# Kernel optimization log

Hardware: AMD Instinct MI355X
Metric: run time of the kernel (lower is better)

The kernel has to match this reference:

```python
import jax, jax.numpy as jnp
import numpy as np

D = 1024  # input_size == context_size

def setup_inputs() -> dict:
    key = jax.random.key(0)
    ks = jax.random.split(key, 8)
    B, S = 16, 4096
    s = 1.0 / np.sqrt(D)
    return {
        "x": jax.random.normal(ks[0], (B, S, D), dtype=jnp.float32),
        "context": jax.random.normal(ks[1], (B, D), dtype=jnp.float32),
        "W_in": jax.random.uniform(ks[2], (D, D), jnp.float32, -s, s),
        "b_in": jax.random.uniform(ks[3], (D,), jnp.float32, -s, s),
        "W_ctx": jax.random.uniform(ks[4], (D, D), jnp.float32, -s, s),
        "b_ctx": jax.random.uniform(ks[5], (D,), jnp.float32, -s, s),
        "w_att": jax.random.uniform(ks[6], (D,), jnp.float32, -s, s),
        "b_att": jax.random.uniform(ks[7], (), jnp.float32, -s, s),
    }

def reference(x, context, W_in, b_in, W_ctx, b_ctx, w_att, b_att):
    # projected_input: [B,S,D]; projected_context: [B,D] broadcast over S
    pi = jnp.einsum('bsd,ed->bse', x, W_in) + b_in
    pc = jnp.einsum('bd,ed->be', context, W_ctx) + b_ctx
    h = jnp.tanh(pi + pc[:, None, :])                      # [B,S,D]
    scores = jnp.einsum('bsd,d->bs', h, w_att) + b_att      # [B,S]
    weights = jax.nn.softmax(scores, axis=1)                # [B,S]
    context_vector = jnp.einsum('bs,bsd->bd', weights, x)   # [B,D]
    # dropout is identity in eval mode
    return context_vector
```

## Files before the change

kernel.cpp:

```cpp
#include <hip/hip_runtime.h>
#include <hip/hip_bf16.h>
#include <math.h>

#define NB 16
#define NS 4096
#define ND 1024
#define NM (NB * NS)

#define WS_T       0
#define WS_SCORES  16384
#define WS_WEIGHTS (WS_SCORES + NB * NS)
#define WS_SHARED  (WS_WEIGHTS + NB * NS)
#define WS_XBF16   (WS_SHARED + 524288)
#define WS_SPART   (WS_XBF16 + 33554432)
#define WS_NEED    (((size_t)WS_SPART + 524288) * 4)

typedef short v8s __attribute__((ext_vector_type(8)));
typedef float v4f __attribute__((ext_vector_type(4)));
typedef unsigned short ushort;

#define G_AS __attribute__((address_space(1)))
#define L_AS __attribute__((address_space(3)))

__device__ __forceinline__ ushort f2bf(float f) {
    __hip_bfloat16 h = __float2bfloat16(f);
    return *reinterpret_cast<ushort*>(&h);
}

__device__ __forceinline__ float bf2f(ushort u) {
    return __uint_as_float(((unsigned)u) << 16);
}

__device__ __forceinline__ float fast_tanh(float x) {
    float e = __expf(2.0f * x);
    return 1.0f - 2.0f / (e + 1.0f);
}

__global__ __launch_bounds__(256) void convw_kernel(const float* __restrict__ W,
                                                    ushort* __restrict__ Wb) {
    int flat = blockIdx.x * 256 + threadIdx.x;
#pragma unroll
    for (int j = 0; j < 2; ++j) {
        int idx = flat + j * 131072;
        float4 v = ((const float4*)W)[idx];
        ushort4 o;
        o.x = f2bf(v.x); o.y = f2bf(v.y); o.z = f2bf(v.z); o.w = f2bf(v.w);
        ((ushort4*)Wb)[idx] = o;
    }
}

__global__ __launch_bounds__(256) void convx_kernel(const float* __restrict__ x,
                                                    ushort* __restrict__ xb) {
    size_t base = (size_t)blockIdx.x * 256 + threadIdx.x;
#pragma unroll
    for (int i = 0; i < 16; ++i) {
        size_t idx8 = base + (size_t)i * 524288;
        float4 a = ((const float4*)x)[idx8 * 2];
        float4 c = ((const float4*)x)[idx8 * 2 + 1];
        v8s o;
        o[0] = (short)f2bf(a.x); o[1] = (short)f2bf(a.y);
        o[2] = (short)f2bf(a.z); o[3] = (short)f2bf(a.w);
        o[4] = (short)f2bf(c.x); o[5] = (short)f2bf(c.y);
        o[6] = (short)f2bf(c.z); o[7] = (short)f2bf(c.w);
        ((v8s*)xb)[idx8] = o;
    }
}

__global__ __launch_bounds__(256) void tvec_kernel(const float* __restrict__ context,
                                                   const float* __restrict__ W_ctx,
                                                   const float* __restrict__ b_in,
                                                   const float* __restrict__ b_ctx,
                                                   float* __restrict__ t) {
    __shared__ float ctx[ND];
    int b = blockIdx.y;
    int tid = threadIdx.x;
    for (int i = tid; i < ND; i += 256) ctx[i] = context[b * ND + i];
    __syncthreads();
    int e = blockIdx.x * 64 + (tid >> 2);
    int kq = tid & 3;
    const float4* wr = (const float4*)(W_ctx + (size_t)e * ND + kq * 256);
    const float4* cr = (const float4*)(ctx + kq * 256);
    float acc = 0.f;
#pragma unroll 4
    for (int k = 0; k < 64; ++k) {
        float4 w = wr[k];
        float4 c = cr[k];
        acc += c.x * w.x + c.y * w.y + c.z * w.z + c.w * w.w;
    }
    acc += __shfl_xor(acc, 1);
    acc += __shfl_xor(acc, 2);
    if (kq == 0) t[b * ND + e] = acc + b_in[e] + b_ctx[e];
}

__global__ __launch_bounds__(512) void scores_tile_kernel(const ushort* __restrict__ xbf,
                                                          const ushort* __restrict__ Wb,
                                                          const float* __restrict__ t,
                                                          const float* __restrict__ w_att,
                                                          float* __restrict__ spart) {
    __shared__ ushort As[2][16384];
    __shared__ ushort Bs[2][16384];
    __shared__ float red[8][128];

    int tid = threadIdx.x;
    int o = blockIdx.x;
    int xcd = o & 7, idx = o >> 3;
    int ct = idx & 3;
    int rt = xcd * 32 + (idx >> 2);
    int row0 = rt << 8;
    int e0 = ct << 8;
    int b = row0 >> 12;

    int scol = ((tid & 7) ^ ((tid >> 3) & 7)) * 8;
    const ushort* gA = xbf + (size_t)(row0 + (tid >> 3)) * ND + scol;
    const ushort* gB = Wb + (size_t)(e0 + (tid >> 3)) * ND + scol;

    int wid = tid >> 6, l = tid & 63;
    int l15 = l & 15, kq4 = l >> 4;
    int l7 = l15 & 7;
    int WM = (wid >> 2) * 128;
    int WN = (wid & 3) * 64;

    v4f acc[8][4];
#pragma unroll
    for (int i = 0; i < 8; ++i)
#pragma unroll
        for (int j = 0; j < 4; ++j) acc[i][j] = (v4f)(0.f);

#define STAGE_A(SB, H, KO)                                                                              \
    {                                                                                                   \
        __builtin_amdgcn_global_load_lds((const G_AS void*)(gA + (size_t)(H) * 128 * ND + (KO)),        \
                                         (L_AS void*)&As[SB][((H) * 1024 + tid) * 8], 16, 0, 0);        \
        __builtin_amdgcn_global_load_lds((const G_AS void*)(gA + (size_t)((H) * 128 + 64) * ND + (KO)), \
                                         (L_AS void*)&As[SB][((H) * 1024 + 512 + tid) * 8], 16, 0, 0);  \
    }
#define STAGE_B(SB, H, KO)                                                                              \
    {                                                                                                   \
        __builtin_amdgcn_global_load_lds((const G_AS void*)(gB + (size_t)(H) * 128 * ND + (KO)),        \
                                         (L_AS void*)&Bs[SB][((H) * 1024 + tid) * 8], 16, 0, 0);        \
        __builtin_amdgcn_global_load_lds((const G_AS void*)(gB + (size_t)((H) * 128 + 64) * ND + (KO)), \
                                         (L_AS void*)&Bs[SB][((H) * 1024 + 512 + tid) * 8], 16, 0, 0);  \
    }

#define PHASE(BUF, KK, MH, STMT)                                                                   \
    {                                                                                              \
        STMT;                                                                                      \
        const int kswz = (((KK) * 4 + kq4) ^ l7) * 8;                                              \
        v8s af[4], bf[4];                                                                          \
        _Pragma("unroll") for (int j = 0; j < 4; ++j)                                              \
            af[j] = *(const v8s*)&As[BUF][(WM + ((MH) * 4 + j) * 16 + l15) * 64 + kswz];           \
        _Pragma("unroll") for (int n = 0; n < 4; ++n)                                              \
            bf[n] = *(const v8s*)&Bs[BUF][(WN + n * 16 + l15) * 64 + kswz];                        \
        __builtin_amdgcn_s_barrier();                                                              \
        __builtin_amdgcn_s_setprio(1);                                                             \
        _Pragma("unroll") for (int j = 0; j < 4; ++j)                                              \
            _Pragma("unroll") for (int n = 0; n < 4; ++n)                                          \
                acc[(MH) * 4 + j][n] = __builtin_amdgcn_mfma_f32_16x16x32_bf16(                    \
                    af[j], bf[n], acc[(MH) * 4 + j][n], 0, 0, 0);                                  \
        __builtin_amdgcn_s_setprio(0);                                                             \
        __builtin_amdgcn_s_barrier();                                                              \
    }

#define KTILE(BUF, SB, KON, DOST)                                  \
    PHASE(BUF, 0, 0, if (DOST) STAGE_A(SB, 0, KON));               \
    PHASE(BUF, 0, 1, if (DOST) STAGE_A(SB, 1, KON));               \
    PHASE(BUF, 1, 0, if (DOST) STAGE_B(SB, 0, KON));               \
    PHASE(BUF, 1, 1, if (DOST) STAGE_B(SB, 1, KON));               \
    asm volatile("s_waitcnt vmcnt(0)" ::: "memory");               \
    __builtin_amdgcn_s_barrier();

    STAGE_A(0, 0, 0);
    STAGE_A(0, 1, 0);
    STAGE_B(0, 0, 0);
    STAGE_B(0, 1, 0);
    asm volatile("s_waitcnt vmcnt(0)" ::: "memory");
    __builtin_amdgcn_s_barrier();

#pragma unroll 1
    for (int it = 0; it < 8; ++it) {
        int kbase = it * 128;
        KTILE(0, 1, kbase + 64, true);
        KTILE(1, 0, kbase + 128, (it < 7));
    }

#undef KTILE
#undef PHASE
#undef STAGE_B
#undef STAGE_A

    float s[8][4];
#pragma unroll
    for (int i = 0; i < 8; ++i)
#pragma unroll
        for (int j = 0; j < 4; ++j) s[i][j] = 0.f;

#pragma unroll
    for (int nf = 0; nf < 4; ++nf) {
        int e = e0 + WN + nf * 16 + l15;
        float tv = t[b * ND + e];
        float wv = w_att[e];
#pragma unroll
        for (int mf = 0; mf < 8; ++mf)
#pragma unroll
            for (int r = 0; r < 4; ++r)
                s[mf][r] += fast_tanh(acc[mf][nf][r] + tv) * wv;
    }
#pragma unroll
    for (int mf = 0; mf < 8; ++mf)
#pragma unroll
        for (int r = 0; r < 4; ++r) {
            float v = s[mf][r];
            v += __shfl_xor(v, 1);
            v += __shfl_xor(v, 2);
            v += __shfl_xor(v, 4);
            v += __shfl_xor(v, 8);
            s[mf][r] = v;
        }
    if (l15 == 0) {
#pragma unroll
        for (int mf = 0; mf < 8; ++mf)
#pragma unroll
            for (int r = 0; r < 4; ++r)
                red[wid][mf * 16 + kq4 * 4 + r] = s[mf][r];
    }
    __syncthreads();
    if (tid < 256) {
        int mg = tid >> 7;
        int rl = tid & 127;
        float v = red[mg * 4 + 0][rl] + red[mg * 4 + 1][rl] +
                  red[mg * 4 + 2][rl] + red[mg * 4 + 3][rl];
        spart[ct * 65536 + row0 + mg * 128 + rl] = v;
    }
}

__global__ __launch_bounds__(512) void scores_mfma_kernel(const float* __restrict__ x,
                                                          const ushort* __restrict__ Wb,
                                                          const float* __restrict__ t,
                                                          const float* __restrict__ w_att,
                                                          float* __restrict__ scores) {
    __shared__ ushort As[2][64 * 256];
    __shared__ float red[8][64];

    int tid = threadIdx.x;
    int row0 = blockIdx.x * 64;
    int b = row0 >> 12;
    const float4* xf4 = (const float4*)x;

    int sr = tid >> 3;
    int sc = tid & 7;
    int swzbase = (sr & 7) << 3;

    float4 nx[8];
#pragma unroll
    for (int j = 0; j < 8; ++j)
        nx[j] = xf4[(size_t)(row0 + sr) * 256 + sc + j * 8];
#pragma unroll
    for (int j = 0; j < 8; ++j) {
        int c4 = sc + j * 8;
        ushort4 o;
        o.x = f2bf(nx[j].x); o.y = f2bf(nx[j].y); o.z = f2bf(nx[j].z); o.w = f2bf(nx[j].w);
        *(ushort4*)&As[0][sr * 256 + ((c4 * 4) ^ swzbase)] = o;
    }
    __syncthreads();

    int w = tid >> 6;
    int l = tid & 63;
    int l15 = l & 15;
    int kofs = (l >> 4) * 8;
    int xorv = (l & 7) << 3;
    int n0 = w * 128;

    v4f acc[2][4][4];
#pragma unroll
    for (int p = 0; p < 2; ++p)
#pragma unroll
        for (int i = 0; i < 4; ++i)
#pragma unroll
            for (int j = 0; j < 4; ++j) acc[p][i][j] = (v4f)(0.f);

    const ushort* bbase0 = Wb + (size_t)(n0 + l15) * ND + kofs;
    const ushort* bbase1 = bbase0 + (size_t)64 * ND;

#pragma unroll
    for (int kh = 0; kh < 4; ++kh) {
        if (kh < 3) {
#pragma unroll
            for (int j = 0; j < 8; ++j)
                nx[j] = xf4[(size_t)(row0 + sr) * 256 + (kh + 1) * 64 + sc + j * 8];
        }
        const ushort* Ab = &As[kh & 1][0];
        int kb = kh * 256;

        v8s b0c[4], b0n[4], b1[4];
#pragma unroll
        for (int nf = 0; nf < 4; ++nf) b0c[nf] = *(const v8s*)(bbase0 + (size_t)nf * 16 * ND + kb);

#pragma unroll
        for (int ks = 0; ks < 8; ++ks) {
            int kk = kb + ks * 32;
            int elem = (ks * 32 + kofs) ^ xorv;
            v8s af[4];
#pragma unroll
            for (int mf = 0; mf < 4; ++mf)
                af[mf] = *(const v8s*)&Ab[(mf * 16 + l15) * 256 + elem];
#pragma unroll
            for (int nf = 0; nf < 4; ++nf)
                b1[nf] = *(const v8s*)(bbase1 + (size_t)nf * 16 * ND + kk);
            if (ks < 7) {
#pragma unroll
                for (int nf = 0; nf < 4; ++nf)
                    b0n[nf] = *(const v8s*)(bbase0 + (size_t)nf * 16 * ND + kk + 32);
            }
#pragma unroll
            for (int mf = 0; mf < 4; ++mf)
#pragma unroll
                for (int nf = 0; nf < 4; ++nf)
                    acc[0][mf][nf] = __builtin_amdgcn_mfma_f32_16x16x32_bf16(
                        af[mf], b0c[nf], acc[0][mf][nf], 0, 0, 0);
#pragma unroll
            for (int mf = 0; mf < 4; ++mf)
#pragma unroll
                for (int nf = 0; nf < 4; ++nf)
                    acc[1][mf][nf] = __builtin_amdgcn_mfma_f32_16x16x32_bf16(
                        af[mf], b1[nf], acc[1][mf][nf], 0, 0, 0);
#pragma unroll
            for (int nf = 0; nf < 4; ++nf) b0c[nf] = b0n[nf];
        }

        if (kh < 3) {
#pragma unroll
            for (int j = 0; j < 8; ++j) {
                int c4 = sc + j * 8;
                ushort4 o;
                o.x = f2bf(nx[j].x); o.y = f2bf(nx[j].y); o.z = f2bf(nx[j].z); o.w = f2bf(nx[j].w);
                *(ushort4*)&As[(kh + 1) & 1][sr * 256 + ((c4 * 4) ^ swzbase)] = o;
            }
            __syncthreads();
        }
    }

    float s[4][4];
#pragma unroll
    for (int i = 0; i < 4; ++i)
#pragma unroll
        for (int j = 0; j < 4; ++j) s[i][j] = 0.f;

#pragma unroll
    for (int pass = 0; pass < 2; ++pass)
#pragma unroll
        for (int nf = 0; nf < 4; ++nf) {
            int e = n0 + pass * 64 + nf * 16 + l15;
            float tv = t[b * ND + e];
            float wv = w_att[e];
#pragma unroll
            for (int mf = 0; mf < 4; ++mf)
#pragma unroll
                for (int r = 0; r < 4; ++r)
                    s[mf][r] += fast_tanh(acc[pass][mf][nf][r] + tv) * wv;
        }

#pragma unroll
    for (int mf = 0; mf < 4; ++mf)
#pragma unroll
        for (int r = 0; r < 4; ++r) {
            float v = s[mf][r];
            v += __shfl_xor(v, 1);
            v += __shfl_xor(v, 2);
            v += __shfl_xor(v, 4);
            v += __shfl_xor(v, 8);
            s[mf][r] = v;
        }
    if (l15 == 0) {
#pragma unroll
        for (int mf = 0; mf < 4; ++mf)
#pragma unroll
            for (int r = 0; r < 4; ++r)
                red[w][mf * 16 + (l >> 4) * 4 + r] = s[mf][r];
    }
    __syncthreads();
    if (tid < 64) {
        float v = 0.f;
#pragma unroll
        for (int ww = 0; ww < 8; ++ww) v += red[ww][tid];
        scores[(size_t)b * NS + (row0 & (NS - 1)) + tid] = v;
    }
}

__global__ __launch_bounds__(256) void softmax4_kernel(const float* __restrict__ spart,
                                                       float* __restrict__ weights) {
    int b = blockIdx.x;
    int tid = threadIdx.x;
    float v[16];
    float lmax = -1e30f;
#pragma unroll
    for (int i = 0; i < 16; ++i) {
        int grow = b * NS + tid + i * 256;
        float sum = 0.f;
#pragma unroll
        for (int c = 0; c < 4; ++c) sum += spart[c * 65536 + grow];
        v[i] = sum;
        lmax = fmaxf(lmax, sum);
    }
#pragma unroll
    for (int off = 32; off >= 1; off >>= 1) lmax = fmaxf(lmax, __shfl_xor(lmax, off));
    __shared__ float redm[4];
    int wave = tid >> 6;
    if ((tid & 63) == 0) redm[wave] = lmax;
    __syncthreads();
    float bmax = fmaxf(fmaxf(redm[0], redm[1]), fmaxf(redm[2], redm[3]));

    float lsum = 0.f;
#pragma unroll
    for (int i = 0; i < 16; ++i) {
        v[i] = expf(v[i] - bmax);
        lsum += v[i];
    }
#pragma unroll
    for (int off = 32; off >= 1; off >>= 1) lsum += __shfl_xor(lsum, off);
    __shared__ float reds[4];
    if ((tid & 63) == 0) reds[wave] = lsum;
    __syncthreads();
    float inv = 1.0f / (reds[0] + reds[1] + reds[2] + reds[3]);
#pragma unroll
    for (int i = 0; i < 16; ++i) weights[b * NS + tid + i * 256] = v[i] * inv;
}

__global__ __launch_bounds__(256) void softmax_kernel(const float* __restrict__ scores,
                                                      float* __restrict__ weights) {
    int b = blockIdx.x;
    int tid = threadIdx.x;
    float v[16];
    float lmax = -1e30f;
#pragma unroll
    for (int i = 0; i < 16; ++i) {
        v[i] = scores[b * NS + tid + i * 256];
        lmax = fmaxf(lmax, v[i]);
    }
#pragma unroll
    for (int off = 32; off >= 1; off >>= 1) lmax = fmaxf(lmax, __shfl_xor(lmax, off));
    __shared__ float redm[4];
    int wave = tid >> 6;
    if ((tid & 63) == 0) redm[wave] = lmax;
    __syncthreads();
    float bmax = fmaxf(fmaxf(redm[0], redm[1]), fmaxf(redm[2], redm[3]));

    float lsum = 0.f;
#pragma unroll
    for (int i = 0; i < 16; ++i) {
        v[i] = expf(v[i] - bmax);
        lsum += v[i];
    }
#pragma unroll
    for (int off = 32; off >= 1; off >>= 1) lsum += __shfl_xor(lsum, off);
    __shared__ float reds[4];
    if ((tid & 63) == 0) reds[wave] = lsum;
    __syncthreads();
    float inv = 1.0f / (reds[0] + reds[1] + reds[2] + reds[3]);
#pragma unroll
    for (int i = 0; i < 16; ++i) weights[b * NS + tid + i * 256] = v[i] * inv;
}

__global__ __launch_bounds__(256) void wsum_kernel(const float* __restrict__ x,
                                                   const float* __restrict__ w,
                                                   float* __restrict__ part) {
    int sc = blockIdx.x, b = blockIdx.y;
    int d0 = threadIdx.x * 4;
    const float* xb = x + ((size_t)b * NS + sc * 128) * ND;
    const float* wb = w + b * NS + sc * 128;
    float4 acc = {0.f, 0.f, 0.f, 0.f};
    for (int ss = 0; ss < 128; ++ss) {
        float wv = wb[ss];
        float4 xv = *(const float4*)&xb[(size_t)ss * ND + d0];
        acc.x += wv * xv.x;
        acc.y += wv * xv.y;
        acc.z += wv * xv.z;
        acc.w += wv * xv.w;
    }
    *(float4*)&part[(size_t)(b * 32 + sc) * ND + d0] = acc;
}

__global__ __launch_bounds__(256) void wsum_bf_kernel(const ushort* __restrict__ xbf,
                                                      const float* __restrict__ w,
                                                      float* __restrict__ part) {
    int sc = blockIdx.x, b = blockIdx.y;
    int d0 = threadIdx.x * 4;
    const ushort* xb = xbf + ((size_t)b * NS + sc * 128) * ND;
    const float* wb = w + b * NS + sc * 128;
    float4 acc = {0.f, 0.f, 0.f, 0.f};
    for (int ss = 0; ss < 128; ++ss) {
        float wv = wb[ss];
        ushort4 xv = *(const ushort4*)&xb[(size_t)ss * ND + d0];
        acc.x += wv * bf2f(xv.x);
        acc.y += wv * bf2f(xv.y);
        acc.z += wv * bf2f(xv.z);
        acc.w += wv * bf2f(xv.w);
    }
    *(float4*)&part[(size_t)(b * 32 + sc) * ND + d0] = acc;
}

__global__ __launch_bounds__(256) void reduce_kernel(const float* __restrict__ part,
                                                     float* __restrict__ out) {
    int b = blockIdx.x;
    int d0 = threadIdx.x * 4;
    float4 acc = {0.f, 0.f, 0.f, 0.f};
#pragma unroll
    for (int sc = 0; sc < 32; ++sc) {
        float4 v = *(const float4*)&part[(size_t)(b * 32 + sc) * ND + d0];
        acc.x += v.x;
        acc.y += v.y;
        acc.z += v.z;
        acc.w += v.w;
    }
    *(float4*)&out[b * ND + d0] = acc;
}

extern "C" void kernel_launch(void* const* d_in, const int* in_sizes, int n_in,
                              void* d_out, int out_size, void* d_ws, size_t ws_size,
                              hipStream_t stream) {
    const float* x       = (const float*)d_in[0];
    const float* context = (const float*)d_in[1];
    const float* W_in    = (const float*)d_in[2];
    const float* b_in    = (const float*)d_in[3];
    const float* W_ctx   = (const float*)d_in[4];
    const float* b_ctx   = (const float*)d_in[5];
    const float* w_att   = (const float*)d_in[6];

    float* ws      = (float*)d_ws;
    float* t       = ws + WS_T;
    float* scores  = ws + WS_SCORES;
    float* weights = ws + WS_WEIGHTS;
    ushort* wbf16  = (ushort*)(ws + WS_SHARED);
    ushort* xbf16  = (ushort*)(ws + WS_XBF16);
    float* spart   = ws + WS_SPART;
    float* partfb  = ws + WS_SHARED;
    float* out     = (float*)d_out;

    bool fast = ws_size >= WS_NEED;

    convw_kernel<<<dim3(512), 256, 0, stream>>>(W_in, wbf16);
    tvec_kernel<<<dim3(16, NB), 256, 0, stream>>>(context, W_ctx, b_in, b_ctx, t);
    if (fast) {
        convx_kernel<<<dim3(2048), 256, 0, stream>>>(x, xbf16);
        scores_tile_kernel<<<dim3(1024), 512, 0, stream>>>(xbf16, wbf16, t, w_att, spart);
        softmax4_kernel<<<dim3(NB), 256, 0, stream>>>(spart, weights);
        wsum_bf_kernel<<<dim3(32, NB), 256, 0, stream>>>(xbf16, weights, spart);
        reduce_kernel<<<dim3(NB), 256, 0, stream>>>(spart, out);
    } else {
        scores_mfma_kernel<<<dim3(NM / 64), 512, 0, stream>>>(x, wbf16, t, w_att, scores);
        softmax_kernel<<<dim3(NB), 256, 0, stream>>>(scores, weights);
        wsum_kernel<<<dim3(32, NB), 256, 0, stream>>>(x, weights, partfb);
        reduce_kernel<<<dim3(NB), 256, 0, stream>>>(partfb, out);
    }
}
```

Before: 310.9 us.

## Restage GEMM LDS layout into k-slices with finer-grained vmcnt pipelining

Reorganizes the shared-memory tiles of the scores GEMM into 32-wide k-slices with a new XOR swizzle, so each global_load_lds stage fills one k-half of a buffer. The main loop is unrolled into eight phases that issue loads for later k-slices and wait only with partial vmcnt counts, replacing the full vmcnt(0) drain after each k-tile. Global loads are now issued after the LDS fragment reads inside each phase. The intent is to keep more memory traffic in flight and overlap it with MFMA work, at the cost of more complex wait bookkeeping that must stay correct.

```diff
diff --git a/kernel.cpp b/kernel.cpp
--- a/kernel.cpp
+++ b/kernel.cpp
@@ -110,13 +110,17 @@
     int e0 = ct << 8;
     int b = row0 >> 12;
 
-    int scol = ((tid & 7) ^ ((tid >> 3) & 7)) * 8;
-    const ushort* gA = xbf + (size_t)(row0 + (tid >> 3)) * ND + scol;
-    const ushort* gB = Wb + (size_t)(e0 + (tid >> 3)) * ND + scol;
+    int srow = tid >> 2;
+    int sg = (srow ^ (srow >> 2)) & 3;
+    int skq = (tid & 3) ^ sg;
+    const ushort* gA0 = xbf + (size_t)(row0 + srow) * ND + skq * 8;
+    const ushort* gA1 = gA0 + (size_t)128 * ND;
+    const ushort* gB0 = Wb + (size_t)(e0 + srow) * ND + skq * 8;
+    const ushort* gB1 = gB0 + (size_t)128 * ND;
 
     int wid = tid >> 6, l = tid & 63;
     int l15 = l & 15, kq4 = l >> 4;
-    int l7 = l15 & 7;
+    int kqg = kq4 ^ ((l15 ^ (l15 >> 2)) & 3);
     int WM = (wid >> 2) * 128;
     int WN = (wid & 3) * 64;
 
@@ -126,30 +130,30 @@
 #pragma unroll
         for (int j = 0; j < 4; ++j) acc[i][j] = (v4f)(0.f);
 
-#define STAGE_A(SB, H, KO)                                                                              \
-    {                                                                                                   \
-        __builtin_amdgcn_global_load_lds((const G_AS void*)(gA + (size_t)(H) * 128 * ND + (KO)),        \
-                                         (L_AS void*)&As[SB][((H) * 1024 + tid) * 8], 16, 0, 0);        \
-        __builtin_amdgcn_global_load_lds((const G_AS void*)(gA + (size_t)((H) * 128 + 64) * ND + (KO)), \
-                                         (L_AS void*)&As[SB][((H) * 1024 + 512 + tid) * 8], 16, 0, 0);  \
-    }
-#define STAGE_B(SB, H, KO)                                                                              \
-    {                                                                                                   \
-        __builtin_amdgcn_global_load_lds((const G_AS void*)(gB + (size_t)(H) * 128 * ND + (KO)),        \
-                                         (L_AS void*)&Bs[SB][((H) * 1024 + tid) * 8], 16, 0, 0);        \
-        __builtin_amdgcn_global_load_lds((const G_AS void*)(gB + (size_t)((H) * 128 + 64) * ND + (KO)), \
-                                         (L_AS void*)&Bs[SB][((H) * 1024 + 512 + tid) * 8], 16, 0, 0);  \
-    }
-
-#define PHASE(BUF, KK, MH, STMT)                                                                   \
+#define STG(MAT, BUF, TK, S)                                                                       \
     {                                                                                              \
-        STMT;                                                                                      \
-        const int kswz = (((KK) * 4 + kq4) ^ l7) * 8;                                              \
+        __builtin_amdgcn_global_load_lds((const G_AS void*)(g##MAT##0 + (TK) + (S) * 32),          \
+                                         (L_AS void*)&MAT##s[BUF][((S) * 1024 + tid) * 8], 16, 0, 0); \
+        __builtin_amdgcn_global_load_lds((const G_AS void*)(g##MAT##1 + (TK) + (S) * 32),          \
+                                         (L_AS void*)&MAT##s[BUF][((S) * 1024 + 512 + tid) * 8], 16, 0, 0); \
+    }
+
+#define VM8 asm volatile("s_waitcnt vmcnt(8)" ::: "memory")
+#define VM4 asm volatile("s_waitcnt vmcnt(4)" ::: "memory")
+#define VM0 asm volatile("s_waitcnt vmcnt(0)" ::: "memory")
+#define NOSTG
+#define NOWAIT
+
+#define PHASE(BUF, KK, MH, STAGE_STMT, WAIT_STMT)                                                  \
+    {                                                                                              \
         v8s af[4], bf[4];                                                                          \
         _Pragma("unroll") for (int j = 0; j < 4; ++j)                                              \
-            af[j] = *(const v8s*)&As[BUF][(WM + ((MH) * 4 + j) * 16 + l15) * 64 + kswz];           \
+            af[j] = *(const v8s*)&As[BUF][((KK) * 1024 +                                           \
+                        (WM + ((MH) * 4 + j) * 16 + l15) * 4 + kqg) * 8];                          \
         _Pragma("unroll") for (int n = 0; n < 4; ++n)                                              \
-            bf[n] = *(const v8s*)&Bs[BUF][(WN + n * 16 + l15) * 64 + kswz];                        \
+            bf[n] = *(const v8s*)&Bs[BUF][((KK) * 1024 +                                           \
+                        (WN + n * 16 + l15) * 4 + kqg) * 8];                                       \
+        STAGE_STMT;                                                                                \
         __builtin_amdgcn_s_barrier();                                                              \
         __builtin_amdgcn_s_setprio(1);                                                             \
         _Pragma("unroll") for (int j = 0; j < 4; ++j)                                              \
@@ -157,35 +161,49 @@
                 acc[(MH) * 4 + j][n] = __builtin_amdgcn_mfma_f32_16x16x32_bf16(                    \
                     af[j], bf[n], acc[(MH) * 4 + j][n], 0, 0, 0);                                  \
         __builtin_amdgcn_s_setprio(0);                                                             \
+        WAIT_STMT;                                                                                 \
         __builtin_amdgcn_s_barrier();                                                              \
     }
 
-#define KTILE(BUF, SB, KON, DOST)                                  \
-    PHASE(BUF, 0, 0, if (DOST) STAGE_A(SB, 0, KON));               \
-    PHASE(BUF, 0, 1, if (DOST) STAGE_A(SB, 1, KON));               \
-    PHASE(BUF, 1, 0, if (DOST) STAGE_B(SB, 0, KON));               \
-    PHASE(BUF, 1, 1, if (DOST) STAGE_B(SB, 1, KON));               \
-    asm volatile("s_waitcnt vmcnt(0)" ::: "memory");               \
+    STG(A, 0, 0, 0);
+    STG(B, 0, 0, 0);
+    STG(A, 0, 0, 1);
+    STG(B, 0, 0, 1);
+    STG(A, 1, 64, 0);
+    STG(B, 1, 64, 0);
+    VM4;
     __builtin_amdgcn_s_barrier();
 
-    STAGE_A(0, 0, 0);
-    STAGE_A(0, 1, 0);
-    STAGE_B(0, 0, 0);
-    STAGE_B(0, 1, 0);
-    asm volatile("s_waitcnt vmcnt(0)" ::: "memory");
-    __builtin_amdgcn_s_barrier();
-
 #pragma unroll 1
-    for (int it = 0; it < 8; ++it) {
-        int kbase = it * 128;
-        KTILE(0, 1, kbase + 64, true);
-        KTILE(1, 0, kbase + 128, (it < 7));
-    }
-
-#undef KTILE
+    for (int it = 0; it < 7; ++it) {
+        int tk1 = (2 * it + 1) * 64;
+        int tk2 = (2 * it + 2) * 64;
+        int tk3 = (2 * it + 3) * 64;
+        PHASE(0, 0, 0, STG(A, 1, tk1, 1), NOWAIT)
+        PHASE(0, 0, 1, STG(B, 1, tk1, 1), VM8)
+        PHASE(0, 1, 0, STG(A, 0, tk2, 0), NOWAIT)
+        PHASE(0, 1, 1, STG(B, 0, tk2, 0), VM8)
+        PHASE(1, 0, 0, STG(A, 0, tk2, 1), NOWAIT)
+        PHASE(1, 0, 1, STG(B, 0, tk2, 1), VM8)
+        PHASE(1, 1, 0, STG(A, 1, tk3, 0), NOWAIT)
+        PHASE(1, 1, 1, STG(B, 1, tk3, 0), VM8)
+    }
+    PHASE(0, 0, 0, STG(A, 1, 15 * 64, 1), NOWAIT)
+    PHASE(0, 0, 1, STG(B, 1, 15 * 64, 1), VM8)
+    PHASE(0, 1, 0, NOSTG, NOWAIT)
+    PHASE(0, 1, 1, NOSTG, VM4)
+    PHASE(1, 0, 0, NOSTG, NOWAIT)
+    PHASE(1, 0, 1, NOSTG, VM0)
+    PHASE(1, 1, 0, NOSTG, NOWAIT)
+    PHASE(1, 1, 1, NOSTG, NOWAIT)
+
 #undef PHASE
-#undef STAGE_B
-#undef STAGE_A
+#undef NOWAIT
+#undef NOSTG
+#undef VM0
+#undef VM4
+#undef VM8
+#undef STG
 
     float s[8][4];
 #pragma unroll
```

After: 302.2 us. 1.03x faster.
